# Kernel tuning notes

Measured on AMD Instinct MI355X. Metric: run time of the kernel, lower is better.

## Reference

```python
import jax, jax.numpy as jnp
import numpy as np

VOCAB = 50000
E = 128      # embedding_dim (== hidden so layer weights stack)
H = 128      # hidden_features
L = 2        # n_layers
B = 256      # batch
T = 2048     # seq_len


def setup_inputs() -> dict:
    key = jax.random.key(0)
    ks = jax.random.split(key, 8)
    s = 1.0 / np.sqrt(H)
    x = jax.random.randint(ks[0], (B, T), 0, VOCAB)
    lengths = jax.random.randint(ks[1], (B,), 1, T + 1)
    emb = jax.random.normal(ks[2], (VOCAB, E), jnp.float32) * 0.1
    W_ih = jax.random.uniform(ks[3], (L, H, H), jnp.float32, -s, s)
    W_hh = jax.random.uniform(ks[4], (L, H, H), jnp.float32, -s, s)
    b = jax.random.uniform(ks[5], (L, H), jnp.float32, -s, s)
    cls_w = jax.random.uniform(ks[6], (H, 1), jnp.float32, -s, s)
    cls_b = jnp.zeros((1,), jnp.float32)
    return {"x": x, "lengths": lengths, "emb": emb, "W_ih": W_ih,
            "W_hh": W_hh, "b": b, "cls_w": cls_w, "cls_b": cls_b}


def reference(x, lengths, emb, W_ih, W_hh, b, cls_w, cls_b):
    # x: [B, T] right-padded token ids; lengths: [B] valid lengths.
    ex = emb[x]                       # [B, T, E]
    xs = jnp.moveaxis(ex, 1, 0)       # [T, B, E]
    seq = x.shape[1]
    mask = jnp.arange(seq)[:, None] < lengths[None, :]  # [T, B] alive at step t

    n_layers = W_ih.shape[0]

    def step(hid, inp):
        # hid: [L, B, H]; packed-RNN semantics: only alive rows update.
        tok, m = inp                  # [B, E], [B]
        h_in = tok
        new = []
        for l in range(n_layers):
            h = jnp.tanh(h_in @ W_ih[l] + hid[l] @ W_hh[l] + b[l])
            h = jnp.where(m[:, None], h, hid[l])
            new.append(h)
            h_in = h
        return jnp.stack(new), None

    hid0 = jnp.zeros((n_layers, x.shape[0], W_hh.shape[-1]), emb.dtype)
    hid, _ = jax.lax.scan(step, hid0, (xs, mask))
    # final hidden of last layer -> single-logit sigmoid classifier
    out = jax.nn.sigmoid(hid[-1] @ cls_w + cls_b)  # [B, 1]
    return out
```

## Files before the change

### kernel.cpp

```cpp
#include <hip/hip_runtime.h>
#include <math.h>

#define BATCH 256
#define SEQ   2048
#define HID   128
#define NTHR  512
#define VOCAB 50000

typedef _Float16 v2h __attribute__((ext_vector_type(2)));
typedef _Float16 v8h __attribute__((ext_vector_type(8)));
typedef float    v4f __attribute__((ext_vector_type(4)));

template<int CTRL>
__device__ __forceinline__ float dpp_movf(float x) {
    return __builtin_bit_cast(float,
        __builtin_amdgcn_update_dpp(0, __builtin_bit_cast(int, x),
                                    CTRL, 0xF, 0xF, false));
}
__device__ __forceinline__ float quad_reduce(float x) {
    x += dpp_movf<0xB1>(x);
    x += dpp_movf<0x4E>(x);
    return x;
}
__device__ __forceinline__ float fast_rcp(float x) { return __builtin_amdgcn_rcpf(x); }
__device__ __forceinline__ float fast_tanh(float z) {
    float e = __expf(2.0f * z);
    return 1.0f - 2.0f * fast_rcp(e + 1.0f);
}
__device__ __forceinline__ float dot2(v2h a, v2h b, float c) {
    return __builtin_amdgcn_fdot2(a, b, c, false);
}
#define BCH(u) __builtin_bit_cast(v2h, (u))
#define BC8(u) __builtin_bit_cast(v8h, (u))

__global__ __launch_bounds__(NTHR, 2) void emb_proj_kernel(
    const float* __restrict__ emb,
    const float* __restrict__ W_ih,
    const float* __restrict__ bias,
    _Float16*    __restrict__ Y)
{
    const int tid  = threadIdx.x;
    const int wave = tid >> 6;
    const int lane = tid & 63;
    const int j    = wave * 16 + (lane >> 2);
    const int q    = lane & 3;

    __shared__ __align__(16) _Float16 xr[HID];

    v2h w[16];
#pragma unroll
    for (int i = 0; i < 16; ++i) {
        const int k = q * 32 + 2 * i;
        w[i] = v2h{(_Float16)W_ih[k * HID + j], (_Float16)W_ih[(k + 1) * HID + j]};
    }
    const float bj = bias[j];
    const float4* embf4 = (const float4*)emb;

    for (int r = blockIdx.x; r < VOCAB; r += gridDim.x) {
        if (tid < 32) {
            float4 v = embf4[(size_t)r * 32 + tid];
            uint a01 = __builtin_bit_cast(uint, __builtin_amdgcn_cvt_pkrtz(v.x, v.y));
            uint a23 = __builtin_bit_cast(uint, __builtin_amdgcn_cvt_pkrtz(v.z, v.w));
            ((uint2*)&xr[0])[tid] = uint2{a01, a23};
        }
        __syncthreads();
        const uint4* xp = (const uint4*)&xr[0] + q * 4;
        float acc = 0.f;
#pragma unroll
        for (int i = 0; i < 4; ++i) {
            const uint4 xu = xp[i];
            acc = dot2(BCH(xu.x), w[4*i+0], acc);
            acc = dot2(BCH(xu.y), w[4*i+1], acc);
            acc = dot2(BCH(xu.z), w[4*i+2], acc);
            acc = dot2(BCH(xu.w), w[4*i+3], acc);
        }
        acc = quad_reduce(acc) + bj;
        if (q == 0) Y[(size_t)r * HID + j] = (_Float16)acc;
        __syncthreads();
    }
}

__global__ __launch_bounds__(NTHR, 2) void rnn_mfma_kernel(
    const int*      __restrict__ x,
    const int*      __restrict__ lengths,
    const _Float16* __restrict__ Y,
    const float*    __restrict__ W_ih,
    const float*    __restrict__ W_hh,
    const float*    __restrict__ bias,
    const float*    __restrict__ cls_w,
    const float*    __restrict__ cls_b,
    float*          __restrict__ out)
{
    const int b    = blockIdx.x;
    const int tid  = threadIdx.x;
    const int wave = tid >> 6;
    const int lane = tid & 63;
    const int kg   = lane >> 4;
    const int jcol = wave * 16 + (lane & 15);

    __shared__ int xids[SEQ];
    __shared__ __align__(16) _Float16 h0h[2][HID];
    __shared__ __align__(16) _Float16 h1h[2][HID];
    __shared__ __align__(16) float    red[HID];

    const int len   = lengths[b];
    const int lenm1 = len - 1;
    const float LOG2E2 = 2.88539008177793f;

    for (int i = tid; i < SEQ; i += NTHR) xids[i] = x[b * SEQ + i];
    if (tid < HID) {
        h0h[0][tid] = (_Float16)0.f; h0h[1][tid] = (_Float16)0.f;
        h1h[0][tid] = (_Float16)0.f; h1h[1][tid] = (_Float16)0.f;
    }

    v8h Bhh0[4], Bih1[4], Bhh1[4];
#pragma unroll
    for (int kt = 0; kt < 4; ++kt) {
        v8h b0v, b1v, b2v;
#pragma unroll
        for (int e = 0; e < 8; ++e) {
            const int k = kt * 32 + kg * 8 + e;
            b0v[e] = (_Float16)W_hh[k * HID + jcol];
            b1v[e] = (_Float16)W_ih[HID * HID + k * HID + jcol];
            b2v[e] = (_Float16)W_hh[HID * HID + k * HID + jcol];
        }
        Bhh0[kt] = b0v; Bih1[kt] = b1v; Bhh1[kt] = b2v;
    }
    const float b1K = bias[HID + jcol] * LOG2E2;

    __syncthreads();

    _Float16 zA = Y[(size_t)xids[0] * HID + jcol];
    _Float16 zB = Y[(size_t)xids[min(1, lenm1)] * HID + jcol];

    int ph = 0, pf = 0;

#define TANH_PRE(ZK) (1.0f - 2.0f * fast_rcp(__builtin_amdgcn_exp2f(ZK) + 1.0f))

#define DO_PHASE(RD, WR, ZREG)                                              \
    {                                                                       \
        const uint4* h0p = (const uint4*)&h0h[RD][0];                       \
        const uint4* h1p = (const uint4*)&h1h[RD][0];                       \
        v8h A0[4], A1[4];                                                   \
        _Pragma("unroll")                                                   \
        for (int kt = 0; kt < 4; ++kt) {                                    \
            A0[kt] = BC8(h0p[kt * 4 + kg]);                                 \
            A1[kt] = BC8(h1p[kt * 4 + kg]);                                 \
        }                                                                   \
        const float zcK = (float)ZREG * LOG2E2;      \
        {                                                                   \
            const int tn = xids[min(ph + 2, lenm1)];                        \
            ZREG = Y[(size_t)tn * HID + jcol];                              \
        }                                                                   \
        v4f c0[4], cA[4], cB[4];                                            \
        _Pragma("unroll")                                                   \
        for (int kt = 0; kt < 4; ++kt) {                                    \
            c0[kt] = __builtin_amdgcn_mfma_f32_16x16x32_f16(A0[kt], Bhh0[kt], v4f{0,0,0,0}, 0, 0, 0); \
            cA[kt] = __builtin_amdgcn_mfma_f32_16x16x32_f16(A0[kt], Bih1[kt], v4f{0,0,0,0}, 0, 0, 0); \
            cB[kt] = __builtin_amdgcn_mfma_f32_16x16x32_f16(A1[kt], Bhh1[kt], v4f{0,0,0,0}, 0, 0, 0); \
        }                                                                   \
        const float s0 = (c0[0].x + c0[1].x) + (c0[2].x + c0[3].x);         \
        const float s1 = ((cA[0].x + cA[1].x) + (cA[2].x + cA[3].x))        \
                       + ((cB[0].x + cB[1].x) + (cB[2].x + cB[3].x));       \
        const float t0 = TANH_PRE(__builtin_fmaf(s0, LOG2E2, zcK));         \
        const float t1 = TANH_PRE(__builtin_fmaf(s1, LOG2E2, b1K));         \
        if (kg == 0) {                                                      \
            if (ph < len) h0h[WR][jcol] = (_Float16)t0;                     \
            if (ph >= 1)  h1h[WR][jcol] = (_Float16)t1;                     \
        }                                                                   \
        __syncthreads();                                                    \
    }

    for (;;) {
        DO_PHASE(0, 1, zA)
        ++ph;
        if (ph > len) { pf = 1; break; }
        DO_PHASE(1, 0, zB)
        ++ph;
        if (ph > len) { pf = 0; break; }
    }
#undef DO_PHASE
#undef TANH_PRE

    if (tid < HID) red[tid] = (float)h1h[pf][tid] * cls_w[tid];
    __syncthreads();
    if (tid == 0) {
        float s = 0.f;
        for (int i = 0; i < HID; ++i) s += red[i];
        s += cls_b[0];
        out[b] = fast_rcp(1.0f + __expf(-s));
    }
}

extern "C" void kernel_launch(void* const* d_in, const int* in_sizes, int n_in,
                              void* d_out, int out_size, void* d_ws, size_t ws_size,
                              hipStream_t stream) {
    const int*   x       = (const int*)  d_in[0];
    const int*   lengths = (const int*)  d_in[1];
    const float* emb     = (const float*)d_in[2];
    const float* W_ih    = (const float*)d_in[3];
    const float* W_hh    = (const float*)d_in[4];
    const float* bias    = (const float*)d_in[5];
    const float* cls_w   = (const float*)d_in[6];
    const float* cls_b   = (const float*)d_in[7];
    float*       out     = (float*)      d_out;

    _Float16* Yws = (_Float16*)d_ws;

    emb_proj_kernel<<<2048, NTHR, 0, stream>>>(emb, W_ih, bias, Yws);
    rnn_mfma_kernel<<<BATCH, NTHR, 0, stream>>>(
        x, lengths, Yws, W_ih, W_hh, bias, cls_w, cls_b, out);
}
```

Before: 860.3 us.

## Replace MFMA recurrence step with per-thread dot2 reductions on fewer threads

The sequential RNN kernel drops the 16x16x32 MFMA tiles for the recurrent matvecs. Each thread now holds weights for two output columns over a 32-wide k slice in packed fp16 registers and accumulates with fdot2. A DPP quad reduction then lets each of the four lanes finish a different column or layer output. The block shrinks from 512 to 256 threads, aiming to cut per-step latency and barrier cost in this latency-bound recurrence, at the cost of longer serial dot2 chains per thread.

```diff
diff --git a/kernel.cpp b/kernel.cpp
--- a/kernel.cpp
+++ b/kernel.cpp
@@ -4,12 +4,10 @@
 #define BATCH 256
 #define SEQ   2048
 #define HID   128
-#define NTHR  512
+#define NTHR  256
 #define VOCAB 50000
 
 typedef _Float16 v2h __attribute__((ext_vector_type(2)));
-typedef _Float16 v8h __attribute__((ext_vector_type(8)));
-typedef float    v4f __attribute__((ext_vector_type(4)));
 
 template<int CTRL>
 __device__ __forceinline__ float dpp_movf(float x) {
@@ -23,17 +21,12 @@
     return x;
 }
 __device__ __forceinline__ float fast_rcp(float x) { return __builtin_amdgcn_rcpf(x); }
-__device__ __forceinline__ float fast_tanh(float z) {
-    float e = __expf(2.0f * z);
-    return 1.0f - 2.0f * fast_rcp(e + 1.0f);
-}
 __device__ __forceinline__ float dot2(v2h a, v2h b, float c) {
     return __builtin_amdgcn_fdot2(a, b, c, false);
 }
 #define BCH(u) __builtin_bit_cast(v2h, (u))
-#define BC8(u) __builtin_bit_cast(v8h, (u))
-
-__global__ __launch_bounds__(NTHR, 2) void emb_proj_kernel(
+
+__global__ __launch_bounds__(512, 2) void emb_proj_kernel(
     const float* __restrict__ emb,
     const float* __restrict__ W_ih,
     const float* __restrict__ bias,
@@ -80,7 +73,7 @@
     }
 }
 
-__global__ __launch_bounds__(NTHR, 2) void rnn_mfma_kernel(
+__global__ __launch_bounds__(NTHR, 1) void rnn_dot2_kernel(
     const int*      __restrict__ x,
     const int*      __restrict__ lengths,
     const _Float16* __restrict__ Y,
@@ -95,8 +88,11 @@
     const int tid  = threadIdx.x;
     const int wave = tid >> 6;
     const int lane = tid & 63;
-    const int kg   = lane >> 4;
-    const int jcol = wave * 16 + (lane & 15);
+    const int jg   = wave * 16 + (lane >> 2);
+    const int q    = lane & 3;
+    const int jm   = lane & 1;
+    const int isl1 = (lane >> 1) & 1;
+    const int jt   = 2 * jg + jm;
 
     __shared__ int xids[SEQ];
     __shared__ __align__(16) _Float16 h0h[2][HID];
@@ -113,25 +109,27 @@
         h1h[0][tid] = (_Float16)0.f; h1h[1][tid] = (_Float16)0.f;
     }
 
-    v8h Bhh0[4], Bih1[4], Bhh1[4];
-#pragma unroll
-    for (int kt = 0; kt < 4; ++kt) {
-        v8h b0v, b1v, b2v;
-#pragma unroll
-        for (int e = 0; e < 8; ++e) {
-            const int k = kt * 32 + kg * 8 + e;
-            b0v[e] = (_Float16)W_hh[k * HID + jcol];
-            b1v[e] = (_Float16)W_ih[HID * HID + k * HID + jcol];
-            b2v[e] = (_Float16)W_hh[HID * HID + k * HID + jcol];
+    v2h whh0[2][16], wih1[2][16], whh1[2][16];
+#pragma unroll
+    for (int i = 0; i < 16; ++i) {
+        const int k = 32 * q + 2 * i;
+#pragma unroll
+        for (int m = 0; m < 2; ++m) {
+            const int j = 2 * jg + m;
+            whh0[m][i] = v2h{(_Float16)W_hh[k * HID + j],
+                             (_Float16)W_hh[(k + 1) * HID + j]};
+            wih1[m][i] = v2h{(_Float16)W_ih[HID * HID + k * HID + j],
+                             (_Float16)W_ih[HID * HID + (k + 1) * HID + j]};
+            whh1[m][i] = v2h{(_Float16)W_hh[HID * HID + k * HID + j],
+                             (_Float16)W_hh[HID * HID + (k + 1) * HID + j]};
         }
-        Bhh0[kt] = b0v; Bih1[kt] = b1v; Bhh1[kt] = b2v;
-    }
-    const float b1K = bias[HID + jcol] * LOG2E2;
+    }
+    const float b1K = bias[HID + jt] * LOG2E2;
 
     __syncthreads();
 
-    _Float16 zA = Y[(size_t)xids[0] * HID + jcol];
-    _Float16 zB = Y[(size_t)xids[min(1, lenm1)] * HID + jcol];
+    _Float16 zA = Y[(size_t)xids[0] * HID + jt];
+    _Float16 zB = Y[(size_t)xids[min(1, lenm1)] * HID + jt];
 
     int ph = 0, pf = 0;
 
@@ -139,35 +137,54 @@
 
 #define DO_PHASE(RD, WR, ZREG)                                              \
     {                                                                       \
-        const uint4* h0p = (const uint4*)&h0h[RD][0];                       \
-        const uint4* h1p = (const uint4*)&h1h[RD][0];                       \
-        v8h A0[4], A1[4];                                                   \
-        _Pragma("unroll")                                                   \
-        for (int kt = 0; kt < 4; ++kt) {                                    \
-            A0[kt] = BC8(h0p[kt * 4 + kg]);                                 \
-            A1[kt] = BC8(h1p[kt * 4 + kg]);                                 \
-        }                                                                   \
-        const float zcK = (float)ZREG * LOG2E2;      \
+        const uint4* h0p = (const uint4*)&h0h[RD][0] + q * 4;               \
+        const uint4* h1p = (const uint4*)&h1h[RD][0] + q * 4;               \
+        const float zcK = (float)ZREG * LOG2E2;                             \
         {                                                                   \
             const int tn = xids[min(ph + 2, lenm1)];                        \
-            ZREG = Y[(size_t)tn * HID + jcol];                              \
+            ZREG = Y[(size_t)tn * HID + jt];                                \
         }                                                                   \
-        v4f c0[4], cA[4], cB[4];                                            \
+        float a0_0 = 0.f, a0_1 = 0.f;             \
+        float aA_0 = 0.f, aA_1 = 0.f;                        \
+        float aB_0 = 0.f, aB_1 = 0.f;                        \
         _Pragma("unroll")                                                   \
-        for (int kt = 0; kt < 4; ++kt) {                                    \
-            c0[kt] = __builtin_amdgcn_mfma_f32_16x16x32_f16(A0[kt], Bhh0[kt], v4f{0,0,0,0}, 0, 0, 0); \
-            cA[kt] = __builtin_amdgcn_mfma_f32_16x16x32_f16(A0[kt], Bih1[kt], v4f{0,0,0,0}, 0, 0, 0); \
-            cB[kt] = __builtin_amdgcn_mfma_f32_16x16x32_f16(A1[kt], Bhh1[kt], v4f{0,0,0,0}, 0, 0, 0); \
+        for (int c = 0; c < 4; ++c) {                                       \
+            const uint4 hu = h0p[c];                                        \
+            const uint4 gu = h1p[c];                                        \
+            a0_0 = dot2(BCH(hu.x), whh0[0][4*c+0], a0_0);                   \
+            a0_0 = dot2(BCH(hu.y), whh0[0][4*c+1], a0_0);                   \
+            a0_0 = dot2(BCH(hu.z), whh0[0][4*c+2], a0_0);                   \
+            a0_0 = dot2(BCH(hu.w), whh0[0][4*c+3], a0_0);                   \
+            a0_1 = dot2(BCH(hu.x), whh0[1][4*c+0], a0_1);                   \
+            a0_1 = dot2(BCH(hu.y), whh0[1][4*c+1], a0_1);                   \
+            a0_1 = dot2(BCH(hu.z), whh0[1][4*c+2], a0_1);                   \
+            a0_1 = dot2(BCH(hu.w), whh0[1][4*c+3], a0_1);                   \
+            aA_0 = dot2(BCH(hu.x), wih1[0][4*c+0], aA_0);                   \
+            aA_0 = dot2(BCH(hu.y), wih1[0][4*c+1], aA_0);                   \
+            aA_0 = dot2(BCH(hu.z), wih1[0][4*c+2], aA_0);                   \
+            aA_0 = dot2(BCH(hu.w), wih1[0][4*c+3], aA_0);                   \
+            aA_1 = dot2(BCH(hu.x), wih1[1][4*c+0], aA_1);                   \
+            aA_1 = dot2(BCH(hu.y), wih1[1][4*c+1], aA_1);                   \
+            aA_1 = dot2(BCH(hu.z), wih1[1][4*c+2], aA_1);                   \
+            aA_1 = dot2(BCH(hu.w), wih1[1][4*c+3], aA_1);                   \
+            aB_0 = dot2(BCH(gu.x), whh1[0][4*c+0], aB_0);                   \
+            aB_0 = dot2(BCH(gu.y), whh1[0][4*c+1], aB_0);                   \
+            aB_0 = dot2(BCH(gu.z), whh1[0][4*c+2], aB_0);                   \
+            aB_0 = dot2(BCH(gu.w), whh1[0][4*c+3], aB_0);                   \
+            aB_1 = dot2(BCH(gu.x), whh1[1][4*c+0], aB_1);                   \
+            aB_1 = dot2(BCH(gu.y), whh1[1][4*c+1], aB_1);                   \
+            aB_1 = dot2(BCH(gu.z), whh1[1][4*c+2], aB_1);                   \
+            aB_1 = dot2(BCH(gu.w), whh1[1][4*c+3], aB_1);                   \
         }                                                                   \
-        const float s0 = (c0[0].x + c0[1].x) + (c0[2].x + c0[3].x);         \
-        const float s1 = ((cA[0].x + cA[1].x) + (cA[2].x + cA[3].x))        \
-                       + ((cB[0].x + cB[1].x) + (cB[2].x + cB[3].x));       \
-        const float t0 = TANH_PRE(__builtin_fmaf(s0, LOG2E2, zcK));         \
-        const float t1 = TANH_PRE(__builtin_fmaf(s1, LOG2E2, b1K));         \
-        if (kg == 0) {                                                      \
-            if (ph < len) h0h[WR][jcol] = (_Float16)t0;                     \
-            if (ph >= 1)  h1h[WR][jcol] = (_Float16)t1;                     \
-        }                                                                   \
+        float s0_0 = quad_reduce(a0_0);                                     \
+        float s0_1 = quad_reduce(a0_1);                                     \
+        float s1_0 = quad_reduce(aA_0 + aB_0);                              \
+        float s1_1 = quad_reduce(aA_1 + aB_1);                              \
+        const float sj  = jm  ? (isl1 ? s1_1 : s0_1) : (isl1 ? s1_0 : s0_0);\
+        const float cj  = isl1 ? b1K : zcK;                                 \
+        const float t   = TANH_PRE(__builtin_fmaf(sj, LOG2E2, cj));         \
+        if (!isl1) { if (ph < len) h0h[WR][jt] = (_Float16)t; }             \
+        else       { if (ph >= 1)  h1h[WR][jt] = (_Float16)t; }             \
         __syncthreads();                                                    \
     }
 
@@ -207,7 +224,7 @@
 
     _Float16* Yws = (_Float16*)d_ws;
 
-    emb_proj_kernel<<<2048, NTHR, 0, stream>>>(emb, W_ih, bias, Yws);
-    rnn_mfma_kernel<<<BATCH, NTHR, 0, stream>>>(
+    emb_proj_kernel<<<2048, 512, 0, stream>>>(emb, W_ih, bias, Yws);
+    rnn_dot2_kernel<<<BATCH, NTHR, 0, stream>>>(
         x, lengths, Yws, W_ih, W_hh, bias, cls_w, cls_b, out);
 }
```

New measurement: 818.1 us. 4.9% less time.
